# Performance work log

Measured on AMD Instinct MI355X. Metric: run time of the kernel, lower is better.

## Reference

```python
import jax, jax.numpy as jnp
import numpy as np

N = 50000
E = 800000
IN_DIM = 10
EMB = 32
HID = 128
LAYERS = 3
BN_EPS = 1e-5


def setup_inputs() -> dict:
    key = jax.random.key(0)
    ks = jax.random.split(key, 16)
    inp = {}
    inp["x"] = jax.random.normal(ks[0], (N, IN_DIM), dtype=jnp.float32)
    inp["edge_index"] = jax.random.randint(ks[1], (2, E), 0, N, dtype=jnp.int64)
    inp["edge_weight"] = jax.random.uniform(ks[2], (E,), dtype=jnp.float32)
    # learned parameters
    inp["emb_table"] = jax.random.normal(ks[3], (N, EMB), dtype=jnp.float32) * 0.02
    inp["ft_W"] = jax.random.normal(ks[4], (EMB, IN_DIM), dtype=jnp.float32) * 0.05
    inp["ft_b"] = jnp.zeros((EMB,), dtype=jnp.float32)
    inp["comb_W"] = jax.random.normal(ks[5], (HID, 2 * EMB), dtype=jnp.float32) * 0.05
    inp["comb_b"] = jnp.zeros((HID,), dtype=jnp.float32)
    inp["conv_W"] = jax.random.normal(ks[6], (LAYERS, HID, HID), dtype=jnp.float32) * 0.05
    inp["conv_b"] = jnp.zeros((LAYERS, HID), dtype=jnp.float32)
    inp["bn_gamma"] = jnp.ones((HID,), dtype=jnp.float32)
    inp["bn_beta"] = jnp.zeros((HID,), dtype=jnp.float32)
    inp["bn_mean"] = jnp.zeros((HID,), dtype=jnp.float32)
    inp["bn_var"] = jnp.ones((HID,), dtype=jnp.float32)
    inp["lin_W"] = jax.random.normal(ks[7], (1, HID), dtype=jnp.float32) * 0.05
    inp["lin_b"] = jnp.zeros((1,), dtype=jnp.float32)
    return inp


def gcn_conv(h, row, col, ew, W, b):
    # PyG GCNConv: x' = D^{-1/2} (A + I) D^{-1/2} x W + b
    n = h.shape[0]
    loop = jnp.arange(n, dtype=row.dtype)
    r = jnp.concatenate([row, loop])          # source nodes
    c = jnp.concatenate([col, loop])          # target nodes
    w = jnp.concatenate([ew, jnp.ones((n,), dtype=ew.dtype)])
    deg = jax.ops.segment_sum(w, c, num_segments=n)
    dinv = jnp.where(deg > 0, jax.lax.rsqrt(deg), 0.0)
    norm = dinv[r] * w * dinv[c]               # [E+N]
    xt = h @ W.T                                # [N, HID]
    msg = xt[r] * norm[:, None]                 # gather + scale
    out = jax.ops.segment_sum(msg, c, num_segments=n)
    return out + b


def reference(x, edge_index, edge_weight, emb_table, ft_W, ft_b, comb_W, comb_b,
              conv_W, conv_b, bn_gamma, bn_beta, bn_mean, bn_var, lin_W, lin_b):
    x = jnp.nan_to_num(x, nan=0.0)
    node_emb = emb_table                        # embedding(arange(N)) == full table
    feat_emb = x @ ft_W.T + ft_b
    combined = jnp.concatenate([node_emb, feat_emb], axis=1)
    h = jax.nn.relu(combined @ comb_W.T + comb_b)
    # dropout disabled (eval mode)
    row, col = edge_index[0], edge_index[1]
    inv_std = jax.lax.rsqrt(bn_var + BN_EPS)
    for i in range(LAYERS):
        h_new = gcn_conv(h, row, col, edge_weight, conv_W[i], conv_b[i])
        h_new = jax.nn.relu(h_new)
        h_new = (h_new - bn_mean) * inv_std * bn_gamma + bn_beta  # BN eval mode
        h = h_new + h                            # residual (shapes always match)
    out = h @ lin_W.T + lin_b
    return jnp.clip(out, -10.0, 10.0)
```

## Files before the change

### kernel.cpp

```cpp
#include <hip/hip_runtime.h>
#include <hip/hip_fp16.h>
#include <math.h>

#define NN 50000
#define EE 800000
#define INDIM 10
#define EMB 32
#define HID 128
#define NLAYERS 3
#define BN_EPS 1e-5f
#define CAP 64

typedef _Float16 h2v __attribute__((ext_vector_type(2)));
__device__ __forceinline__ float fdot2(__half2 a, __half2 b, float c) {
    return __builtin_amdgcn_fdot2(*(h2v*)&a, *(h2v*)&b, c, false);
}

__device__ __forceinline__ int clampN(int v) {
    return v < 0 ? 0 : (v >= NN ? NN - 1 : v);
}


__global__ void k_init(int* __restrict__ cursor) {
    int i = blockIdx.x * blockDim.x + threadIdx.x;
    if (i < NN) cursor[i] = 0;
}

__global__ void k_fill(const int* __restrict__ ei,
                       const float* __restrict__ ew,
                       int* __restrict__ cursor, unsigned* __restrict__ csr) {
    int e = blockIdx.x * blockDim.x + threadIdx.x;
    if (e < EE) {
        int r = clampN(ei[e]);
        int c = clampN(ei[EE + e]);
        int pos = atomicAdd(&cursor[c], 1);
        if (pos >= CAP) pos = CAP - 1;
        unsigned short hw = __half_as_ushort(__float2half(ew[e]));
        unsigned v = (unsigned)(unsigned short)r | ((unsigned)hw << 16);
        __builtin_nontemporal_store(v, &csr[(size_t)c * CAP + pos]);
    }
}

__global__ __launch_bounds__(256) void k_deg(const unsigned* __restrict__ csr,
                                             const int* __restrict__ cnt,
                                             float* __restrict__ dinv) {
    int n = blockIdx.x * 4 + (threadIdx.x >> 6);
    int l = threadIdx.x & 63;
    if (n >= NN) return;
    int m = cnt[n]; if (m > CAP) m = CAP;
    const unsigned* seg = &csr[(size_t)n * CAP];
    float s = 0.f;
    for (int i = l; i < m; i += 64)
        s += __half2float(__ushort_as_half((unsigned short)(seg[i] >> 16)));
    #pragma unroll
    for (int o = 32; o; o >>= 1) s += __shfl_xor(s, o, 64);
    if (l == 0) dinv[n] = rsqrtf(1.0f + s);
}

__global__ void k_wprep(const float* __restrict__ convW,
                        const float* __restrict__ combW,
                        __half2* __restrict__ Wtp, float* __restrict__ Wct) {
    int idx = blockIdx.x * blockDim.x + threadIdx.x;
    const int NWT = NLAYERS * 64 * HID;
    if (idx < NWT) {
        int L = idx / (64 * HID);
        int rem = idx - L * 64 * HID;
        int kk = rem >> 7, c = rem & 127;
        const float* Wl = convW + L * HID * HID + c * HID;
        Wtp[idx] = __floats2half2_rn(Wl[2 * kk], Wl[2 * kk + 1]);
    } else {
        int j = idx - NWT;
        if (j < HID * 2 * EMB) {
            int k = j >> 7, c = j & 127;
            Wct[j] = combW[c * (2 * EMB) + k];
        }
    }
}


__global__ __launch_bounds__(256) void k_init_h(
        const float* __restrict__ x, const float* __restrict__ emb,
        const float* __restrict__ ftW, const float* __restrict__ ftb,
        const float* __restrict__ Wct, const float* __restrict__ combb,
        float* __restrict__ h) {
    __shared__ float csh[64 * 68];
    __shared__ float xsh[64 * INDIM];
    int t = threadIdx.x;
    int n0 = blockIdx.x * 64;

    for (int s = t; s < 64 * INDIM; s += 256) {
        int j = s / INDIM, q = s - j * INDIM;
        float xv = (n0 + j < NN) ? x[(n0 + j) * INDIM + q] : 0.f;
        unsigned bits = __float_as_uint(xv) & 0x7fffffffu;
        if (bits > 0x7f800000u) xv = 0.f;
        xsh[s] = xv;
    }
    #pragma unroll
    for (int i = 0; i < 8; ++i) {
        int s = i * 256 + t;
        int j = s >> 5, k = s & 31;
        csh[j * 68 + k] = (n0 + j < NN) ? emb[(n0 + j) * EMB + k] : 0.f;
    }
    __syncthreads();
    #pragma unroll
    for (int i = 0; i < 8; ++i) {
        int s = i * 256 + t;
        int j = s >> 5, kk = s & 31;
        float acc = ftb[kk];
        #pragma unroll
        for (int q = 0; q < INDIM; ++q)
            acc = fmaf(ftW[kk * INDIM + q], xsh[j * INDIM + q], acc);
        csh[j * 68 + 32 + kk] = acc;
    }
    __syncthreads();

    int ty = t >> 4, tx = t & 15;
    float acc[4][8];
    #pragma unroll
    for (int i = 0; i < 4; ++i)
        #pragma unroll
        for (int j = 0; j < 8; ++j) acc[i][j] = 0.f;

    for (int k0 = 0; k0 < 64; k0 += 4) {
        float wf[4][8];
        #pragma unroll
        for (int kk = 0; kk < 4; ++kk) {
            float4 a = *(const float4*)&Wct[(k0 + kk) * HID + tx * 8];
            float4 b = *(const float4*)&Wct[(k0 + kk) * HID + tx * 8 + 4];
            wf[kk][0] = a.x; wf[kk][1] = a.y; wf[kk][2] = a.z; wf[kk][3] = a.w;
            wf[kk][4] = b.x; wf[kk][5] = b.y; wf[kk][6] = b.z; wf[kk][7] = b.w;
        }
        float hf[4][4];
        #pragma unroll
        for (int i = 0; i < 4; ++i) {
            float4 hv = *(const float4*)&csh[(ty * 4 + i) * 68 + k0];
            hf[i][0] = hv.x; hf[i][1] = hv.y; hf[i][2] = hv.z; hf[i][3] = hv.w;
        }
        #pragma unroll
        for (int i = 0; i < 4; ++i)
            #pragma unroll
            for (int kk = 0; kk < 4; ++kk)
                #pragma unroll
                for (int j = 0; j < 8; ++j)
                    acc[i][j] = fmaf(hf[i][kk], wf[kk][j], acc[i][j]);
    }
    #pragma unroll
    for (int i = 0; i < 4; ++i) {
        int n = n0 + ty * 4 + i;
        if (n < NN) {
            float b0 = combb[tx * 8],     b1 = combb[tx * 8 + 1];
            float b2 = combb[tx * 8 + 2], b3 = combb[tx * 8 + 3];
            float b4 = combb[tx * 8 + 4], b5 = combb[tx * 8 + 5];
            float b6 = combb[tx * 8 + 6], b7 = combb[tx * 8 + 7];
            *(float4*)&h[(size_t)n * HID + tx * 8] = make_float4(
                fmaxf(acc[i][0] + b0, 0.f), fmaxf(acc[i][1] + b1, 0.f),
                fmaxf(acc[i][2] + b2, 0.f), fmaxf(acc[i][3] + b3, 0.f));
            *(float4*)&h[(size_t)n * HID + tx * 8 + 4] = make_float4(
                fmaxf(acc[i][4] + b4, 0.f), fmaxf(acc[i][5] + b5, 0.f),
                fmaxf(acc[i][6] + b6, 0.f), fmaxf(acc[i][7] + b7, 0.f));
        }
    }
}


#define BM 64
__global__ __launch_bounds__(256) void k_gemm(const float* __restrict__ h,
                                              const __half2* __restrict__ Wtp,
                                              const float* __restrict__ dinv,
                                              __half* __restrict__ xt) {
    __shared__ __half2 hsh[BM * 66];
    int t = threadIdx.x;
    int row0 = blockIdx.x * BM;
    #pragma unroll
    for (int i = 0; i < 8; ++i) {
        int s = i * 256 + t;
        int r = s >> 5;
        int cc = s & 31;
        float4 v = make_float4(0.f, 0.f, 0.f, 0.f);
        int row = row0 + r;
        if (row < NN) v = *(const float4*)&h[row * HID + cc * 4];
        hsh[r * 66 + cc * 2]     = __floats2half2_rn(v.x, v.y);
        hsh[r * 66 + cc * 2 + 1] = __floats2half2_rn(v.z, v.w);
    }
    __syncthreads();
    int ty = t >> 4, tx = t & 15;
    float acc[4][8];
    #pragma unroll
    for (int i = 0; i < 4; ++i)
        #pragma unroll
        for (int j = 0; j < 8; ++j) acc[i][j] = 0.f;

    #pragma unroll 2
    for (int k2 = 0; k2 < 64; ++k2) {
        const __half2* wr = &Wtp[k2 * HID + tx * 8];
        __half2 wf[8];
        *(float4*)&wf[0] = *(const float4*)&wr[0];
        *(float4*)&wf[4] = *(const float4*)&wr[4];
        __half2 hf[4];
        #pragma unroll
        for (int i = 0; i < 4; ++i) hf[i] = hsh[(ty * 4 + i) * 66 + k2];
        #pragma unroll
        for (int i = 0; i < 4; ++i)
            #pragma unroll
            for (int j = 0; j < 8; ++j)
                acc[i][j] = fdot2(hf[i], wf[j], acc[i][j]);
    }
    #pragma unroll
    for (int i = 0; i < 4; ++i) {
        int row = row0 + ty * 4 + i;
        if (row < NN) {
            float dv = dinv[row];
            __half2 p0 = __floats2half2_rn(acc[i][0] * dv, acc[i][1] * dv);
            __half2 p1 = __floats2half2_rn(acc[i][2] * dv, acc[i][3] * dv);
            __half2 p2 = __floats2half2_rn(acc[i][4] * dv, acc[i][5] * dv);
            __half2 p3 = __floats2half2_rn(acc[i][6] * dv, acc[i][7] * dv);
            uint4 u = make_uint4(*(unsigned*)&p0, *(unsigned*)&p1,
                                 *(unsigned*)&p2, *(unsigned*)&p3);
            *(uint4*)&xt[(size_t)row * HID + tx * 8] = u;
        }
    }
}


__global__ __launch_bounds__(256) void k_aggregate(
        const __half* __restrict__ xt, float* __restrict__ h,
        const int* __restrict__ cnt, const unsigned* __restrict__ csr,
        const float* __restrict__ dinv,
        const float* __restrict__ bias, const float* __restrict__ gamma,
        const float* __restrict__ beta, const float* __restrict__ mean,
        const float* __restrict__ var,
        const float* __restrict__ linW, const float* __restrict__ linb,
        float* __restrict__ out, int last) {
    int n = blockIdx.x * 4 + (threadIdx.x >> 6);
    int l = threadIdx.x & 63;
    if (n >= NN) return;
    const __half2* xt2 = (const __half2*)xt;
    const unsigned* seg = &csr[(size_t)n * CAP];
    int m = cnt[n]; if (m > CAP) m = CAP;
    float2 accA = make_float2(0.f, 0.f);
    float2 accB = make_float2(0.f, 0.f);
    int i = 0;
    for (; i + 7 < m; i += 8) {
        unsigned p_[8];
        #pragma unroll
        for (int q = 0; q < 8; ++q) p_[q] = seg[i + q];
        __half2 r_[8];
        #pragma unroll
        for (int q = 0; q < 8; ++q)
            r_[q] = xt2[(size_t)(p_[q] & 0xffffu) * 64 + l];
        #pragma unroll
        for (int q = 0; q < 8; ++q) {
            float wq = __half2float(__ushort_as_half((unsigned short)(p_[q] >> 16)));
            float2 v = __half22float2(r_[q]);
            if (q & 1) { accB.x = fmaf(v.x, wq, accB.x); accB.y = fmaf(v.y, wq, accB.y); }
            else       { accA.x = fmaf(v.x, wq, accA.x); accA.y = fmaf(v.y, wq, accA.y); }
        }
    }
    for (; i < m; ++i) {
        unsigned p = seg[i];
        float wgt = __half2float(__ushort_as_half((unsigned short)(p >> 16)));
        float2 v = __half22float2(xt2[(size_t)(p & 0xffffu) * 64 + l]);
        accA.x = fmaf(v.x, wgt, accA.x); accA.y = fmaf(v.y, wgt, accA.y);
    }
    float dn = dinv[n];
    float2 vs = __half22float2(xt2[(size_t)n * 64 + l]);
    float ax = (accA.x + accB.x + vs.x) * dn;
    float ay = (accA.y + accB.y + vs.y) * dn;

    int c0 = 2 * l, c1 = c0 + 1;
    float v0 = fmaxf(ax + bias[c0], 0.f);
    float v1 = fmaxf(ay + bias[c1], 0.f);
    v0 = (v0 - mean[c0]) * rsqrtf(var[c0] + BN_EPS) * gamma[c0] + beta[c0];
    v1 = (v1 - mean[c1]) * rsqrtf(var[c1] + BN_EPS) * gamma[c1] + beta[c1];
    float2 hv = *(const float2*)&h[(size_t)n * HID + c0];
    float2 outv = make_float2(v0 + hv.x, v1 + hv.y);
    if (!last) {
        *(float2*)&h[(size_t)n * HID + c0] = outv;
    } else {
        float2 wv = *(const float2*)&linW[c0];
        float s = outv.x * wv.x + outv.y * wv.y;
        #pragma unroll
        for (int o = 32; o; o >>= 1) s += __shfl_xor(s, o, 64);
        if (l == 0) {
            float o = s + linb[0];
            out[n] = fminf(fmaxf(o, -10.f), 10.f);
        }
    }
}


extern "C" void kernel_launch(void* const* d_in, const int* in_sizes, int n_in,
                              void* d_out, int out_size, void* d_ws, size_t ws_size,
                              hipStream_t stream) {
    const float* x     = (const float*)d_in[0];
    const int*   ei    = (const int*)d_in[1];
    const float* ew    = (const float*)d_in[2];
    const float* emb   = (const float*)d_in[3];
    const float* ftW   = (const float*)d_in[4];
    const float* ftb   = (const float*)d_in[5];
    const float* combW = (const float*)d_in[6];
    const float* combb = (const float*)d_in[7];
    const float* convW = (const float*)d_in[8];
    const float* convb = (const float*)d_in[9];
    const float* gamma = (const float*)d_in[10];
    const float* beta  = (const float*)d_in[11];
    const float* mean  = (const float*)d_in[12];
    const float* var   = (const float*)d_in[13];
    const float* linW  = (const float*)d_in[14];
    const float* linb  = (const float*)d_in[15];
    float* out = (float*)d_out;

    char* ws = (char*)d_ws;
    size_t off = 0;
    auto alloc = [&](size_t bytes) {
        void* p = ws + off;
        off = (off + bytes + 255) & ~(size_t)255;
        return p;
    };
    float*    h    = (float*)alloc((size_t)NN * HID * 4);
    __half*   xt   = (__half*)alloc((size_t)NN * HID * 2);
    float*    dinv = (float*)alloc((size_t)NN * 4);
    int*      cnt  = (int*)alloc((size_t)NN * 4);
    unsigned* csr  = (unsigned*)alloc((size_t)NN * CAP * 4);
    __half2*  Wtp  = (__half2*)alloc((size_t)NLAYERS * 64 * HID * 4);
    float*    Wct  = (float*)alloc((size_t)HID * 2 * EMB * 4);

    const int NBK = (NN + 255) / 256;
    const int EB = (EE + 255) / 256;
    const int NODE4 = (NN + 3) / 4;
    const int IHB = (NN + 63) / 64;
    const int WPB = (NLAYERS * 64 * HID + HID * 2 * EMB + 255) / 256;

    k_init<<<NBK, 256, 0, stream>>>(cnt);
    k_fill<<<EB, 256, 0, stream>>>(ei, ew, cnt, csr);
    k_deg<<<NODE4, 256, 0, stream>>>(csr, cnt, dinv);
    k_wprep<<<WPB, 256, 0, stream>>>(convW, combW, Wtp, Wct);
    k_init_h<<<IHB, 256, 0, stream>>>(x, emb, ftW, ftb, Wct, combb, h);
    for (int L = 0; L < NLAYERS; ++L) {
        k_gemm<<<(NN + BM - 1) / BM, 256, 0, stream>>>(h, Wtp + (size_t)L * 64 * HID, dinv, xt);
        k_aggregate<<<NODE4, 256, 0, stream>>>(xt, h, cnt, csr, dinv,
                                               convb + L * HID, gamma, beta, mean, var,
                                               linW, linb, out, L == NLAYERS - 1);
    }
}
```

Before: 323.7 us.

## Aggregate one node per 16 lanes with 16-byte gathers

Restructures the GCN aggregation kernel so each node is handled by 16 threads instead of a full 64-lane wavefront. Each thread gathers a 16-byte chunk (8 fp16 features) per neighbor and accumulates 8 channels. The aim is fewer, wider memory transactions and four nodes per wavefront, which cuts per-edge index loads and instruction overhead. The unroll drops to 4 neighbors, which leaves less memory-level parallelism per thread. The final reduction shrinks to a 16-lane shuffle.

New measurement: 303.9 us. 6.1% less time.

```diff
diff --git a/kernel.cpp b/kernel.cpp
--- a/kernel.cpp
+++ b/kernel.cpp
@@ -18,6 +18,16 @@
 
 __device__ __forceinline__ int clampN(int v) {
     return v < 0 ? 0 : (v >= NN ? NN - 1 : v);
+}
+
+__device__ __forceinline__ void accum8(float acc[8], float4 v, float w) {
+    const __half2* hh = (const __half2*)&v;
+    #pragma unroll
+    for (int k = 0; k < 4; ++k) {
+        float2 f = __half22float2(hh[k]);
+        acc[2 * k]     = fmaf(f.x, w, acc[2 * k]);
+        acc[2 * k + 1] = fmaf(f.y, w, acc[2 * k + 1]);
+    }
 }
 
 
@@ -231,57 +241,63 @@
         const float* __restrict__ var,
         const float* __restrict__ linW, const float* __restrict__ linb,
         float* __restrict__ out, int last) {
-    int n = blockIdx.x * 4 + (threadIdx.x >> 6);
-    int l = threadIdx.x & 63;
+    int g = threadIdx.x >> 4, q = threadIdx.x & 15;
+    int n = blockIdx.x * 16 + g;
     if (n >= NN) return;
-    const __half2* xt2 = (const __half2*)xt;
+    const float4* xt4 = (const float4*)xt;
     const unsigned* seg = &csr[(size_t)n * CAP];
     int m = cnt[n]; if (m > CAP) m = CAP;
-    float2 accA = make_float2(0.f, 0.f);
-    float2 accB = make_float2(0.f, 0.f);
+    float acc[8];
+    #pragma unroll
+    for (int j = 0; j < 8; ++j) acc[j] = 0.f;
     int i = 0;
-    for (; i + 7 < m; i += 8) {
-        unsigned p_[8];
-        #pragma unroll
-        for (int q = 0; q < 8; ++q) p_[q] = seg[i + q];
-        __half2 r_[8];
-        #pragma unroll
-        for (int q = 0; q < 8; ++q)
-            r_[q] = xt2[(size_t)(p_[q] & 0xffffu) * 64 + l];
-        #pragma unroll
-        for (int q = 0; q < 8; ++q) {
-            float wq = __half2float(__ushort_as_half((unsigned short)(p_[q] >> 16)));
-            float2 v = __half22float2(r_[q]);
-            if (q & 1) { accB.x = fmaf(v.x, wq, accB.x); accB.y = fmaf(v.y, wq, accB.y); }
-            else       { accA.x = fmaf(v.x, wq, accA.x); accA.y = fmaf(v.y, wq, accA.y); }
-        }
+    for (; i + 3 < m; i += 4) {
+        unsigned p0 = seg[i],     p1 = seg[i + 1];
+        unsigned p2 = seg[i + 2], p3 = seg[i + 3];
+        float4 r0 = xt4[(size_t)(p0 & 0xffffu) * 16 + q];
+        float4 r1 = xt4[(size_t)(p1 & 0xffffu) * 16 + q];
+        float4 r2 = xt4[(size_t)(p2 & 0xffffu) * 16 + q];
+        float4 r3 = xt4[(size_t)(p3 & 0xffffu) * 16 + q];
+        float w0 = __half2float(__ushort_as_half((unsigned short)(p0 >> 16)));
+        float w1 = __half2float(__ushort_as_half((unsigned short)(p1 >> 16)));
+        float w2 = __half2float(__ushort_as_half((unsigned short)(p2 >> 16)));
+        float w3 = __half2float(__ushort_as_half((unsigned short)(p3 >> 16)));
+        accum8(acc, r0, w0);
+        accum8(acc, r1, w1);
+        accum8(acc, r2, w2);
+        accum8(acc, r3, w3);
     }
     for (; i < m; ++i) {
         unsigned p = seg[i];
-        float wgt = __half2float(__ushort_as_half((unsigned short)(p >> 16)));
-        float2 v = __half22float2(xt2[(size_t)(p & 0xffffu) * 64 + l]);
-        accA.x = fmaf(v.x, wgt, accA.x); accA.y = fmaf(v.y, wgt, accA.y);
-    }
+        float4 r = xt4[(size_t)(p & 0xffffu) * 16 + q];
+        float w = __half2float(__ushort_as_half((unsigned short)(p >> 16)));
+        accum8(acc, r, w);
+    }
+    accum8(acc, xt4[(size_t)n * 16 + q], 1.0f);
     float dn = dinv[n];
-    float2 vs = __half22float2(xt2[(size_t)n * 64 + l]);
-    float ax = (accA.x + accB.x + vs.x) * dn;
-    float ay = (accA.y + accB.y + vs.y) * dn;
-
-    int c0 = 2 * l, c1 = c0 + 1;
-    float v0 = fmaxf(ax + bias[c0], 0.f);
-    float v1 = fmaxf(ay + bias[c1], 0.f);
-    v0 = (v0 - mean[c0]) * rsqrtf(var[c0] + BN_EPS) * gamma[c0] + beta[c0];
-    v1 = (v1 - mean[c1]) * rsqrtf(var[c1] + BN_EPS) * gamma[c1] + beta[c1];
-    float2 hv = *(const float2*)&h[(size_t)n * HID + c0];
-    float2 outv = make_float2(v0 + hv.x, v1 + hv.y);
+
+    int c0 = q * 8;
+    float hres[8];
+    *(float4*)&hres[0] = *(const float4*)&h[(size_t)n * HID + c0];
+    *(float4*)&hres[4] = *(const float4*)&h[(size_t)n * HID + c0 + 4];
+    float outv[8];
+    #pragma unroll
+    for (int j = 0; j < 8; ++j) {
+        float v = fmaxf(acc[j] * dn + bias[c0 + j], 0.f);
+        v = (v - mean[c0 + j]) * rsqrtf(var[c0 + j] + BN_EPS) * gamma[c0 + j]
+            + beta[c0 + j];
+        outv[j] = v + hres[j];
+    }
     if (!last) {
-        *(float2*)&h[(size_t)n * HID + c0] = outv;
+        *(float4*)&h[(size_t)n * HID + c0]     = *(float4*)&outv[0];
+        *(float4*)&h[(size_t)n * HID + c0 + 4] = *(float4*)&outv[4];
     } else {
-        float2 wv = *(const float2*)&linW[c0];
-        float s = outv.x * wv.x + outv.y * wv.y;
-        #pragma unroll
-        for (int o = 32; o; o >>= 1) s += __shfl_xor(s, o, 64);
-        if (l == 0) {
+        float s = 0.f;
+        #pragma unroll
+        for (int j = 0; j < 8; ++j) s = fmaf(outv[j], linW[c0 + j], s);
+        #pragma unroll
+        for (int o = 8; o; o >>= 1) s += __shfl_xor(s, o, 64);
+        if (q == 0) {
             float o = s + linb[0];
             out[n] = fminf(fmaxf(o, -10.f), 10.f);
         }
@@ -328,6 +344,7 @@
     const int NBK = (NN + 255) / 256;
     const int EB = (EE + 255) / 256;
     const int NODE4 = (NN + 3) / 4;
+    const int AGB = (NN + 15) / 16;
     const int IHB = (NN + 63) / 64;
     const int WPB = (NLAYERS * 64 * HID + HID * 2 * EMB + 255) / 256;
 
@@ -338,8 +355,8 @@
     k_init_h<<<IHB, 256, 0, stream>>>(x, emb, ftW, ftb, Wct, combb, h);
     for (int L = 0; L < NLAYERS; ++L) {
         k_gemm<<<(NN + BM - 1) / BM, 256, 0, stream>>>(h, Wtp + (size_t)L * 64 * HID, dinv, xt);
-        k_aggregate<<<NODE4, 256, 0, stream>>>(xt, h, cnt, csr, dinv,
-                                               convb + L * HID, gamma, beta, mean, var,
-                                               linW, linb, out, L == NLAYERS - 1);
-    }
-}
+        k_aggregate<<<AGB, 256, 0, stream>>>(xt, h, cnt, csr, dinv,
+                                             convb + L * HID, gamma, beta, mean, var,
+                                             linW, linb, out, L == NLAYERS - 1);
+    }
+}
```
